# Performance work log

Measured on AMD Instinct MI355X. Metric: run time of the kernel, lower is better.

Reference implementation:

```python
import jax, jax.numpy as jnp
import numpy as np

T, B, I, H = 512, 512, 128, 512

def setup_inputs() -> dict:
    key = jax.random.key(0)
    ks = jax.random.split(key, 10)
    s = 0.05  # small init scale to avoid gate saturation
    return {
        "x": jax.random.normal(ks[0], (T, B, I), jnp.float32),
        "enc_hiddens": jax.random.normal(ks[1], (1, B, H), jnp.float32),
        "h0": jax.random.normal(ks[2], (1, B, H), jnp.float32) * s,
        "c0": jax.random.normal(ks[3], (1, B, H), jnp.float32) * s,
        "W_ih": jax.random.normal(ks[4], (4 * H, I), jnp.float32) * s,
        "W_hh": jax.random.normal(ks[5], (4 * H, H), jnp.float32) * s,
        "b_ih": jax.random.normal(ks[6], (4 * H,), jnp.float32) * s,
        "b_hh": jax.random.normal(ks[7], (4 * H,), jnp.float32) * s,
        "fc_W": jax.random.normal(ks[8], (I, H), jnp.float32) * s,
        "fc_b": jax.random.normal(ks[9], (I,), jnp.float32) * s,
    }

def reference(x, enc_hiddens, h0, c0, W_ih, W_hh, b_ih, b_hh, fc_W, fc_b):
    # RECURSIVE decoding branch: feed own output back in; store outputs reversed.
    seq_len = x.shape[0]
    b = b_ih + b_hh  # fuse biases

    def step(carry, _):
        inp, h, c = carry  # inp:[B,I], h,c:[B,H]
        gates = inp @ W_ih.T + h @ W_hh.T + b  # [B,4H]
        i_g, f_g, g_g, o_g = jnp.split(gates, 4, axis=-1)  # torch gate order i,f,g,o
        i_g = jax.nn.sigmoid(i_g)
        f_g = jax.nn.sigmoid(f_g)
        g_g = jnp.tanh(g_g)
        o_g = jax.nn.sigmoid(o_g)
        c_new = f_g * c + i_g * g_g
        h_new = o_g * jnp.tanh(c_new)
        out = h_new @ fc_W.T + fc_b            # Linear
        out = 2.0 * jax.nn.sigmoid(out) - 1.0  # use_act affine rescale
        return (out, h_new, c_new), out

    init = (x[seq_len - 1], h0[0], c0[0])
    _, outs = jax.lax.scan(step, init, None, length=seq_len)  # [T,B,I], step t stored at index t
    # original writes dec_outs[seq_len - t - 1], i.e. reversed order
    return jnp.flip(outs, axis=0)
```

## Files before the change

### kernel.cpp

```cpp
#include <hip/hip_runtime.h>

typedef unsigned short u16;
typedef unsigned int   u32;
typedef unsigned long long u64;
typedef short v8s __attribute__((ext_vector_type(8)));
typedef float v16f __attribute__((ext_vector_type(16)));
typedef float v2f  __attribute__((ext_vector_type(2)));

#define B_ 512
#define I_ 128
#define H_ 512
#define KK 640
#define NSTEP 512
#define AST 648

__device__ inline u16 f2b(float x){
  union{float f; unsigned u;} v; v.f = x;
  unsigned r = v.u + 0x7fffu + ((v.u >> 16) & 1u);
  return (u16)(r >> 16);
}

__device__ inline float tanh_fast(float x){
  float e = __expf(2.f * x);
  return 1.f - 2.f / (e + 1.f);
}

__device__ inline void bar_lds(){
  asm volatile("s_waitcnt lgkmcnt(0)" ::: "memory");
  __builtin_amdgcn_s_barrier();
  asm volatile("" ::: "memory");
}

__device__ inline u64 ld64(const u16* p){
  return __hip_atomic_load((const u64*)p, __ATOMIC_RELAXED, __HIP_MEMORY_SCOPE_AGENT);
}
__device__ inline void st32(u16* p, u32 v){
  __hip_atomic_store((u32*)p, v, __ATOMIC_RELAXED, __HIP_MEMORY_SCOPE_AGENT);
}
__device__ inline u32 fpoll(const u32* p){
  return __hip_atomic_load(p, __ATOMIC_RELAXED, __HIP_MEMORY_SCOPE_AGENT);
}
__device__ inline void fst(u32* p, u32 v){
  __hip_atomic_store(p, v, __ATOMIC_RELAXED, __HIP_MEMORY_SCOPE_AGENT);
}

__global__ void init_kernel(const float* __restrict__ x, const float* __restrict__ h0,
    const float* __restrict__ Wih, const float* __restrict__ Whh,
    const float* __restrict__ bih, const float* __restrict__ bhh, const float* __restrict__ fcW,
    u16* __restrict__ Wcat, u16* __restrict__ fcWb, float* __restrict__ bsum,
    u16* __restrict__ hb0, u16* __restrict__ outb, u32* __restrict__ flags)
{
  int idx = blockIdx.x * 256 + threadIdx.x;
  if (idx < 1310720) {
    int g = idx / 640, k = idx - g * 640;
    float v = (k < 512) ? Whh[g * 512 + k] : Wih[g * 128 + (k - 512)];
    Wcat[idx] = f2b(v);
  } else if (idx < 1376256) {
    int i = idx - 1310720; fcWb[i] = f2b(fcW[i]);
  } else if (idx < 1378304) {
    int i = idx - 1376256; bsum[i] = bih[i] + bhh[i];
  } else if (idx < 1640448) {
    int i = idx - 1378304; hb0[i] = f2b(h0[i]);
  } else if (idx < 1705984) {
    int i = idx - 1640448; outb[i] = f2b(x[33488896 + i]);
  } else if (idx < 1706240) {
    flags[idx - 1705984] = 0u;
  }
}

__global__ __launch_bounds__(512, 2) void decoder_persist(
    const u16* __restrict__ Wcat, const float* __restrict__ bsum,
    const u16* __restrict__ fcWb, const float* __restrict__ fcb,
    const float* __restrict__ c0,
    u16* __restrict__ hb0, u16* __restrict__ hb1, const u16* __restrict__ outb,
    float* __restrict__ dout, u32* __restrict__ flags)
{
  __shared__ __align__(16) u16  Alds[32 * AST];
  __shared__ __align__(16) float gbuf[4096];

  const int tid  = threadIdx.x;
  const int wid  = tid >> 6, lane = tid & 63;
  const int l31  = lane & 31, q2 = lane >> 5;
  const int mb   = blockIdx.x & 15;
  const int nb   = blockIdx.x >> 4;
  const int R    = mb * 32;
  u32* gf = flags + mb * 16;

  const bool isfc = (wid >= 4);
  const int  wc   = (wid - 4) * 32;

  v8s wfrag[40];
  if (!isfc) {
    const u16* wr = Wcat + (u64)(wid * 512 + nb * 32 + l31) * KK + q2 * 8;
    #pragma unroll
    for (int kc = 0; kc < 40; ++kc) wfrag[kc] = *reinterpret_cast<const v8s*>(wr + kc * 16);
  } else {
    const u16* fr = fcWb + (u64)(wc + l31) * H_ + q2 * 8;
    #pragma unroll
    for (int kc = 0; kc < 32; ++kc) wfrag[kc] = *reinterpret_cast<const v8s*>(fr + kc * 16);
    #pragma unroll
    for (int kc = 32; kc < 40; ++kc) wfrag[kc] = (v8s){0,0,0,0,0,0,0,0};
  }
  const float bias0 = isfc ? fcb[wc + l31] : bsum[wid * 512 + nb * 32 + l31];

  const bool dopred = isfc && (((wc + l31) >> 3) == nb);

  float oreg[16];
  float* dpend = nullptr;

  const int crow = tid >> 4, ccol = (tid * 2) & 31;
  float cv0 = c0[(R + crow) * H_ + nb * 32 + ccol];
  float cv1 = c0[(R + crow) * H_ + nb * 32 + ccol + 1];

  for (int t = 0; t <= NSTEP; ++t) {
    const u16* hsrc = (t & 1) ? hb1 : hb0;

    if (dopred && dpend) {
      #pragma unroll
      for (int r = 0; r < 16; ++r) {
        int row = (r & 3) + 8 * (r >> 2) + 4 * q2;
        __builtin_nontemporal_store(oreg[r], dpend + (R + row) * I_ + wc + l31);
      }
      dpend = nullptr;
    }

    if (t > 0) {
      const u32 tt = (u32)t;
      for (;;) {
        u32 f = fpoll(gf + 2 * wid + (lane & 1));
        if (__all((int)(f >= tt))) break;
      }
      __asm__ volatile("" ::: "memory");
    }

    u64 tmp[8];
    #pragma unroll
    for (int k = 0; k < 8; ++k) {
      int v = k * 64 + lane;
      int row = v >> 4, c16 = v & 15;
      tmp[k] = ld64(hsrc + (R + row) * H_ + wid * 64 + c16 * 4);
    }
    if (!isfc) {
      #pragma unroll
      for (int k = 0; k < 8; ++k) {
        int v = k * 64 + lane;
        int row = v >> 4, c16 = v & 15;
        *reinterpret_cast<u64*>(&Alds[row * AST + wid * 64 + c16 * 4]) = tmp[k];
      }
    }
    if (t == 0) {
      u64 tp2[2];
      #pragma unroll
      for (int u = 0; u < 2; ++u) {
        int v = u * 512 + tid;
        int row = v >> 5, cc = v & 31;
        tp2[u] = ld64(outb + (R + row) * I_ + cc * 4);
      }
      #pragma unroll
      for (int u = 0; u < 2; ++u) {
        int v = u * 512 + tid;
        int row = v >> 5, cc = v & 31;
        *reinterpret_cast<u64*>(&Alds[row * AST + 512 + cc * 4]) = tp2[u];
      }
    }
    bar_lds();

    v16f acc = {0.f,0.f,0.f,0.f,0.f,0.f,0.f,0.f,0.f,0.f,0.f,0.f,0.f,0.f,0.f,0.f};
    const u16* ab = &Alds[l31 * AST + q2 * 8];
    __builtin_amdgcn_s_setprio(1);
    #pragma unroll
    for (int kc = 0; kc < 16; ++kc) {
      v8s a = *reinterpret_cast<const v8s*>(ab + kc * 16);
      acc = __builtin_amdgcn_mfma_f32_32x32x16_bf16(a, wfrag[kc], acc, 0, 0, 0);
    }
    __builtin_amdgcn_s_setprio(0);

    if (isfc) {
      __builtin_amdgcn_sched_barrier(0);
      #pragma unroll
      for (int k = 0; k < 8; ++k) {
        int v = k * 64 + lane;
        int row = v >> 4, c16 = v & 15;
        *reinterpret_cast<u64*>(&Alds[row * AST + wid * 64 + c16 * 4]) = tmp[k];
      }
    }
    bar_lds();

    __builtin_amdgcn_s_setprio(1);
    #pragma unroll
    for (int kc = 16; kc < 32; ++kc) {
      v8s a = *reinterpret_cast<const v8s*>(ab + kc * 16);
      acc = __builtin_amdgcn_mfma_f32_32x32x16_bf16(a, wfrag[kc], acc, 0, 0, 0);
    }
    __builtin_amdgcn_s_setprio(0);

    if (isfc && t > 0) {
      #pragma unroll
      for (int r = 0; r < 16; ++r) {
        int row = (r & 3) + 8 * (r >> 2) + 4 * q2;
        float o = 2.f / (1.f + __expf(-(acc[r] + bias0))) - 1.f;
        oreg[r] = o;
        Alds[row * AST + 512 + wc + l31] = f2b(o);
      }
      dpend = dout + (u64)(NSTEP - t) * (B_ * I_);
    }
    __syncthreads();

    if (t < NSTEP) {
      if (!isfc) {
        __builtin_amdgcn_s_setprio(1);
        #pragma unroll
        for (int kc = 32; kc < 40; ++kc) {
          v8s a = *reinterpret_cast<const v8s*>(ab + kc * 16);
          acc = __builtin_amdgcn_mfma_f32_32x32x16_bf16(a, wfrag[kc], acc, 0, 0, 0);
        }
        __builtin_amdgcn_s_setprio(0);
        #pragma unroll
        for (int r = 0; r < 16; ++r) {
          int row = (r & 3) + 8 * (r >> 2) + 4 * q2;
          float z = acc[r] + bias0;
          float a2 = (wid == 2) ? tanh_fast(z) : 1.f / (1.f + __expf(-z));
          gbuf[wid * 1024 + row * 32 + l31] = a2;
        }
      }
      __syncthreads();

      u16* hdst = (t & 1) ? hb0 : hb1;
      v2f ig = *reinterpret_cast<const v2f*>(&gbuf[       crow * 32 + ccol]);
      v2f fg = *reinterpret_cast<const v2f*>(&gbuf[1024 + crow * 32 + ccol]);
      v2f gg = *reinterpret_cast<const v2f*>(&gbuf[2048 + crow * 32 + ccol]);
      v2f og = *reinterpret_cast<const v2f*>(&gbuf[3072 + crow * 32 + ccol]);
      float cn0 = fg[0] * cv0 + ig[0] * gg[0];
      float cn1 = fg[1] * cv1 + ig[1] * gg[1];
      cv0 = cn0; cv1 = cn1;
      u32 packed = (u32)f2b(og[0] * tanh_fast(cn0)) | ((u32)f2b(og[1] * tanh_fast(cn1)) << 16);
      st32(hdst + (R + crow) * H_ + nb * 32 + ccol, packed);
      __syncthreads();
      __asm__ volatile("" ::: "memory");
      if (tid == 0) fst(gf + nb, (u32)(t + 1));
    }
  }

  if (dopred && dpend) {
    #pragma unroll
    for (int r = 0; r < 16; ++r) {
      int row = (r & 3) + 8 * (r >> 2) + 4 * q2;
      __builtin_nontemporal_store(oreg[r], dpend + (R + row) * I_ + wc + l31);
    }
  }
}

extern "C" void kernel_launch(void* const* d_in, const int* in_sizes, int n_in,
                              void* d_out, int out_size, void* d_ws, size_t ws_size,
                              hipStream_t stream)
{
  const float* x   = (const float*)d_in[0];
  const float* h0  = (const float*)d_in[2];
  const float* c0  = (const float*)d_in[3];
  const float* Wih = (const float*)d_in[4];
  const float* Whh = (const float*)d_in[5];
  const float* bih = (const float*)d_in[6];
  const float* bhh = (const float*)d_in[7];
  const float* fcW = (const float*)d_in[8];
  const float* fcb = (const float*)d_in[9];

  char* p = (char*)d_ws;
  u16*   Wcat  = (u16*)p;   p += 2048LL * 640 * 2;
  u16*   fcWb  = (u16*)p;   p += 128 * 512 * 2;
  float* bsum  = (float*)p; p += 2048 * 4;
  u16*   hb0   = (u16*)p;   p += 512 * 512 * 2;
  u16*   hb1   = (u16*)p;   p += 512 * 512 * 2;
  u16*   outb  = (u16*)p;   p += 512 * 128 * 2;
  u32*   flags = (u32*)p;   p += 256 * 4;
  float* dout  = (float*)d_out;

  init_kernel<<<6666, 256, 0, stream>>>(x, h0, Wih, Whh, bih, bhh, fcW,
                                        Wcat, fcWb, bsum, hb0, outb, flags);
  decoder_persist<<<256, 512, 0, stream>>>(Wcat, bsum, fcWb, fcb, c0,
                                           hb0, hb1, outb, dout, flags);
}
```

Before: 2.812 ms.

## Split gate and FC GEMMs across K halves with paired-wave LDS reduction

Before, four waves computed gate GEMMs and four computed the FC GEMM, with the FC waves writing h into LDS between two barrier-separated halves. Now each wave pair splits the K dimension in half: each wave computes partial gate and FC accumulators over its K half. The partials are exchanged through a new LDS buffer, using per-pair LDS flags instead of block barriers. This is meant to balance MFMA work across all eight waves and remove one block barrier from the serial per-step critical path. In exchange it adds LDS traffic for the partial sums, spin-waits on LDS flags, and more register pressure from two accumulators and split weight fragments.

```diff
diff --git a/kernel.cpp b/kernel.cpp
--- a/kernel.cpp
+++ b/kernel.cpp
@@ -6,6 +6,7 @@
 typedef short v8s __attribute__((ext_vector_type(8)));
 typedef float v16f __attribute__((ext_vector_type(16)));
 typedef float v2f  __attribute__((ext_vector_type(2)));
+typedef float v4f  __attribute__((ext_vector_type(4)));
 
 #define B_ 512
 #define I_ 128
@@ -25,12 +26,6 @@
   return 1.f - 2.f / (e + 1.f);
 }
 
-__device__ inline void bar_lds(){
-  asm volatile("s_waitcnt lgkmcnt(0)" ::: "memory");
-  __builtin_amdgcn_s_barrier();
-  asm volatile("" ::: "memory");
-}
-
 __device__ inline u64 ld64(const u16* p){
   return __hip_atomic_load((const u64*)p, __ATOMIC_RELAXED, __HIP_MEMORY_SCOPE_AGENT);
 }
@@ -42,6 +37,12 @@
 }
 __device__ inline void fst(u32* p, u32 v){
   __hip_atomic_store(p, v, __ATOMIC_RELAXED, __HIP_MEMORY_SCOPE_AGENT);
+}
+__device__ inline u32 lpoll(const u32* p){
+  return __hip_atomic_load(p, __ATOMIC_RELAXED, __HIP_MEMORY_SCOPE_WORKGROUP);
+}
+__device__ inline void lst(u32* p, u32 v){
+  __hip_atomic_store(p, v, __ATOMIC_RELAXED, __HIP_MEMORY_SCOPE_WORKGROUP);
 }
 
 __global__ void init_kernel(const float* __restrict__ x, const float* __restrict__ h0,
@@ -77,6 +78,8 @@
 {
   __shared__ __align__(16) u16  Alds[32 * AST];
   __shared__ __align__(16) float gbuf[4096];
+  __shared__ __align__(16) v4f  xbuf[2048];
+  __shared__ u32 xfl[8];
 
   const int tid  = threadIdx.x;
   const int wid  = tid >> 6, lane = tid & 63;
@@ -86,24 +89,29 @@
   const int R    = mb * 32;
   u32* gf = flags + mb * 16;
 
-  const bool isfc = (wid >= 4);
-  const int  wc   = (wid - 4) * 32;
-
-  v8s wfrag[40];
-  if (!isfc) {
-    const u16* wr = Wcat + (u64)(wid * 512 + nb * 32 + l31) * KK + q2 * 8;
+  const bool islow = (wid < 4);
+  const int  p     = islow ? wid : (wid - 4);
+  const int  kb    = islow ? 0 : 16;
+
+  if (tid < 8) xfl[tid] = 0;
+
+  v8s wG[24], wF[16];
+  {
+    const u16* wr = Wcat + (u64)(p * 512 + nb * 32 + l31) * KK + q2 * 8;
     #pragma unroll
-    for (int kc = 0; kc < 40; ++kc) wfrag[kc] = *reinterpret_cast<const v8s*>(wr + kc * 16);
-  } else {
-    const u16* fr = fcWb + (u64)(wc + l31) * H_ + q2 * 8;
+    for (int kc = 0; kc < 16; ++kc) wG[kc] = *reinterpret_cast<const v8s*>(wr + (kb + kc) * 16);
+    if (!islow) {
+      #pragma unroll
+      for (int kc = 16; kc < 24; ++kc)
+        wG[kc] = *reinterpret_cast<const v8s*>(wr + (kb + kc) * 16);
+    }
+    const u16* fr = fcWb + (u64)(p * 32 + l31) * H_ + q2 * 8;
     #pragma unroll
-    for (int kc = 0; kc < 32; ++kc) wfrag[kc] = *reinterpret_cast<const v8s*>(fr + kc * 16);
-    #pragma unroll
-    for (int kc = 32; kc < 40; ++kc) wfrag[kc] = (v8s){0,0,0,0,0,0,0,0};
+    for (int kc = 0; kc < 16; ++kc) wF[kc] = *reinterpret_cast<const v8s*>(fr + (kb + kc) * 16);
   }
-  const float bias0 = isfc ? fcb[wc + l31] : bsum[wid * 512 + nb * 32 + l31];
-
-  const bool dopred = isfc && (((wc + l31) >> 3) == nb);
+  const float bias0 = islow ? fcb[p * 32 + l31] : bsum[p * 512 + nb * 32 + l31];
+
+  const bool dopred = islow && (((p * 32 + l31) >> 3) == nb);
 
   float oreg[16];
   float* dpend = nullptr;
@@ -119,7 +127,7 @@
       #pragma unroll
       for (int r = 0; r < 16; ++r) {
         int row = (r & 3) + 8 * (r >> 2) + 4 * q2;
-        __builtin_nontemporal_store(oreg[r], dpend + (R + row) * I_ + wc + l31);
+        __builtin_nontemporal_store(oreg[r], dpend + (R + row) * I_ + p * 32 + l31);
       }
       dpend = nullptr;
     }
@@ -133,14 +141,14 @@
       __asm__ volatile("" ::: "memory");
     }
 
-    u64 tmp[8];
-    #pragma unroll
-    for (int k = 0; k < 8; ++k) {
-      int v = k * 64 + lane;
-      int row = v >> 4, c16 = v & 15;
-      tmp[k] = ld64(hsrc + (R + row) * H_ + wid * 64 + c16 * 4);
-    }
-    if (!isfc) {
+    {
+      u64 tmp[8];
+      #pragma unroll
+      for (int k = 0; k < 8; ++k) {
+        int v = k * 64 + lane;
+        int row = v >> 4, c16 = v & 15;
+        tmp[k] = ld64(hsrc + (R + row) * H_ + wid * 64 + c16 * 4);
+      }
       #pragma unroll
       for (int k = 0; k < 8; ++k) {
         int v = k * 64 + lane;
@@ -163,64 +171,75 @@
         *reinterpret_cast<u64*>(&Alds[row * AST + 512 + cc * 4]) = tp2[u];
       }
     }
-    bar_lds();
-
-    v16f acc = {0.f,0.f,0.f,0.f,0.f,0.f,0.f,0.f,0.f,0.f,0.f,0.f,0.f,0.f,0.f,0.f};
+    __syncthreads();
+
+    v16f accG = {0.f,0.f,0.f,0.f,0.f,0.f,0.f,0.f,0.f,0.f,0.f,0.f,0.f,0.f,0.f,0.f};
+    v16f accF = {0.f,0.f,0.f,0.f,0.f,0.f,0.f,0.f,0.f,0.f,0.f,0.f,0.f,0.f,0.f,0.f};
     const u16* ab = &Alds[l31 * AST + q2 * 8];
     __builtin_amdgcn_s_setprio(1);
     #pragma unroll
     for (int kc = 0; kc < 16; ++kc) {
-      v8s a = *reinterpret_cast<const v8s*>(ab + kc * 16);
-      acc = __builtin_amdgcn_mfma_f32_32x32x16_bf16(a, wfrag[kc], acc, 0, 0, 0);
+      v8s a = *reinterpret_cast<const v8s*>(ab + (kb + kc) * 16);
+      accG = __builtin_amdgcn_mfma_f32_32x32x16_bf16(a, wG[kc], accG, 0, 0, 0);
+      accF = __builtin_amdgcn_mfma_f32_32x32x16_bf16(a, wF[kc], accF, 0, 0, 0);
     }
     __builtin_amdgcn_s_setprio(0);
 
-    if (isfc) {
-      __builtin_amdgcn_sched_barrier(0);
-      #pragma unroll
-      for (int k = 0; k < 8; ++k) {
-        int v = k * 64 + lane;
-        int row = v >> 4, c16 = v & 15;
-        *reinterpret_cast<u64*>(&Alds[row * AST + wid * 64 + c16 * 4]) = tmp[k];
-      }
-    }
-    bar_lds();
-
-    __builtin_amdgcn_s_setprio(1);
-    #pragma unroll
-    for (int kc = 16; kc < 32; ++kc) {
-      v8s a = *reinterpret_cast<const v8s*>(ab + kc * 16);
-      acc = __builtin_amdgcn_mfma_f32_32x32x16_bf16(a, wfrag[kc], acc, 0, 0, 0);
-    }
-    __builtin_amdgcn_s_setprio(0);
-
-    if (isfc && t > 0) {
-      #pragma unroll
-      for (int r = 0; r < 16; ++r) {
-        int row = (r & 3) + 8 * (r >> 2) + 4 * q2;
-        float o = 2.f / (1.f + __expf(-(acc[r] + bias0))) - 1.f;
-        oreg[r] = o;
-        Alds[row * AST + 512 + wc + l31] = f2b(o);
-      }
-      dpend = dout + (u64)(NSTEP - t) * (B_ * I_);
+    const u32 tok = (u32)(t + 1);
+    if (islow) {
+      #pragma unroll
+      for (int j = 0; j < 4; ++j)
+        xbuf[(p * 4 + j) * 64 + lane] = (v4f){accG[4*j], accG[4*j+1], accG[4*j+2], accG[4*j+3]};
+      asm volatile("s_waitcnt lgkmcnt(0)" ::: "memory");
+      lst(&xfl[p], tok);
+      while (lpoll(&xfl[4 + p]) < tok) {}
+      __asm__ volatile("" ::: "memory");
+      #pragma unroll
+      for (int j = 0; j < 4; ++j) {
+        v4f q = xbuf[1024 + (p * 4 + j) * 64 + lane];
+        accF[4*j] += q[0]; accF[4*j+1] += q[1]; accF[4*j+2] += q[2]; accF[4*j+3] += q[3];
+      }
+      if (t > 0) {
+        #pragma unroll
+        for (int r = 0; r < 16; ++r) {
+          int row = (r & 3) + 8 * (r >> 2) + 4 * q2;
+          float o = 2.f / (1.f + __expf(-(accF[r] + bias0))) - 1.f;
+          oreg[r] = o;
+          Alds[row * AST + 512 + p * 32 + l31] = f2b(o);
+        }
+        dpend = dout + (u64)(NSTEP - t) * (B_ * I_);
+      }
+    } else {
+      #pragma unroll
+      for (int j = 0; j < 4; ++j)
+        xbuf[1024 + (p * 4 + j) * 64 + lane] = (v4f){accF[4*j], accF[4*j+1], accF[4*j+2], accF[4*j+3]};
+      asm volatile("s_waitcnt lgkmcnt(0)" ::: "memory");
+      lst(&xfl[4 + p], tok);
+      while (lpoll(&xfl[p]) < tok) {}
+      __asm__ volatile("" ::: "memory");
+      #pragma unroll
+      for (int j = 0; j < 4; ++j) {
+        v4f q = xbuf[(p * 4 + j) * 64 + lane];
+        accG[4*j] += q[0]; accG[4*j+1] += q[1]; accG[4*j+2] += q[2]; accG[4*j+3] += q[3];
+      }
     }
     __syncthreads();
 
     if (t < NSTEP) {
-      if (!isfc) {
+      if (!islow) {
         __builtin_amdgcn_s_setprio(1);
         #pragma unroll
-        for (int kc = 32; kc < 40; ++kc) {
-          v8s a = *reinterpret_cast<const v8s*>(ab + kc * 16);
-          acc = __builtin_amdgcn_mfma_f32_32x32x16_bf16(a, wfrag[kc], acc, 0, 0, 0);
+        for (int kc = 16; kc < 24; ++kc) {
+          v8s a = *reinterpret_cast<const v8s*>(ab + (kb + kc) * 16);
+          accG = __builtin_amdgcn_mfma_f32_32x32x16_bf16(a, wG[kc], accG, 0, 0, 0);
         }
         __builtin_amdgcn_s_setprio(0);
         #pragma unroll
         for (int r = 0; r < 16; ++r) {
           int row = (r & 3) + 8 * (r >> 2) + 4 * q2;
-          float z = acc[r] + bias0;
-          float a2 = (wid == 2) ? tanh_fast(z) : 1.f / (1.f + __expf(-z));
-          gbuf[wid * 1024 + row * 32 + l31] = a2;
+          float z = accG[r] + bias0;
+          float a2 = (p == 2) ? tanh_fast(z) : 1.f / (1.f + __expf(-z));
+          gbuf[p * 1024 + row * 32 + l31] = a2;
         }
       }
       __syncthreads();
@@ -245,7 +264,7 @@
     #pragma unroll
     for (int r = 0; r < 16; ++r) {
       int row = (r & 3) + 8 * (r >> 2) + 4 * q2;
-      __builtin_nontemporal_store(oreg[r], dpend + (R + row) * I_ + wc + l31);
+      __builtin_nontemporal_store(oreg[r], dpend + (R + row) * I_ + p * 32 + l31);
     }
   }
 }
```

After: 3.243 ms. 1.15x slower.
